# Kernel optimization log

Hardware: AMD Instinct MI355X
Metric: run time of the kernel (lower is better)

## Reference

```python
import jax, jax.numpy as jnp
import numpy as np

PAD = 200000   # padding index = all_features_num
D = 128        # input_dim (embedding dim)
H = 256        # hidden_dim
K = 15         # item_num (top-k)
M = 4          # multi_head


def _cos(a, b, eps=1e-8):
    # torch.cosine_similarity semantics with eps clamp on norms
    na = jnp.maximum(jnp.linalg.norm(a, axis=-1), eps)
    nb = jnp.maximum(jnp.linalg.norm(b, axis=-1), eps)
    return jnp.sum(a * b, axis=-1) / (na * nb)


def _rnn_input(x, emb):
    # x: [..., T, F] int. Fields :-2 are embedded+summed, field -2 is time.
    t = x[..., -2].astype(jnp.float32)
    dt = jnp.concatenate([jnp.zeros_like(t[..., :1]), jnp.diff(t, axis=-1)], axis=-1)
    e = emb[x[..., :-2]].sum(axis=-2)          # [..., T, D]
    x_self = e[:, 0:1, -1:, :]                  # [B,1,1,D] (self item placed at last slot of session 0)
    return jnp.concatenate([e, dt[..., None]], axis=-1), x_self


def _time_rnn(seq, W, U, b, wt, return_all=False):
    # Time-aware GRU. seq: [N, T, in+1]; last channel is delta-time feeding a decay gate.
    f, dt = seq[..., :-1], seq[..., -1:]
    N = seq.shape[0]
    g_in = jnp.einsum('nti,ij->ntj', f, W) + b   # precompute input projections [N,T,3H]

    def step(h, inp):
        g, d = inp                               # g:[N,3H], d:[N,1]
        decay = jnp.exp(-jax.nn.relu(d * wt))    # time-aware decay of hidden state
        hd = h * decay
        u = hd @ U
        z = jax.nn.sigmoid(g[:, :H] + u[:, :H])
        r = jax.nn.sigmoid(g[:, H:2 * H] + u[:, H:2 * H])
        n = jnp.tanh(g[:, 2 * H:] + r * u[:, 2 * H:])
        h_new = (1.0 - z) * hd + z * n
        return h_new, h_new

    h0 = jnp.zeros((N, H), seq.dtype)
    h_last, hs = jax.lax.scan(step, h0, (jnp.swapaxes(g_in, 0, 1), jnp.swapaxes(dt, 0, 1)))
    return jnp.swapaxes(hs, 0, 1) if return_all else h_last


def setup_inputs() -> dict:
    key = jax.random.key(0)
    ks = jax.random.split(key, 20)
    def n(k, shape, s=0.05):
        return jax.random.normal(k, shape, jnp.float32) * s
    x = jax.random.randint(ks[0], (512, 16, 64, 8), 0, PAD, dtype=jnp.int32)
    x_continuous = jax.random.randint(ks[1], (128, 128, 8), 0, PAD, dtype=jnp.int32)
    self_loc = jax.random.randint(ks[2], (512,), 0, 64, dtype=jnp.int32)
    emb = n(ks[3], (PAD + 1, D)).at[PAD].set(0.0)  # padding_idx row = 0
    return {
        'x': x, 'x_continuous': x_continuous, 'self_loc': self_loc, 'emb': emb,
        'W_rnn': n(ks[4], (2 * D, 3 * H)), 'U_rnn': n(ks[5], (H, 3 * H)), 'b_rnn': n(ks[6], (3 * H,)),
        'wt_rnn': jax.random.uniform(ks[7], (H,), jnp.float32, 0.0, 1e-5),
        'W_c': n(ks[8], (D, 3 * H)), 'U_c': n(ks[9], (H, 3 * H)), 'b_c': n(ks[10], (3 * H,)),
        'wt_c': jax.random.uniform(ks[11], (H,), jnp.float32, 0.0, 1e-5),
        'Wv': n(ks[12], (2 * H, M)), 'bv': n(ks[13], (M,)),
        'W0': n(ks[14], (D + (2 + M) * H, 1024)), 'b0': n(ks[15], (1024,)),
        'W1': n(ks[16], (1024, 512)), 'b1': n(ks[17], (512,)),
        'W2': n(ks[18], (512, 256)), 'b2': n(ks[19], (256,)),
        'Wp': n(jax.random.fold_in(key, 99), (256, 1)), 'bp': jnp.zeros((1,), jnp.float32),
    }


def reference(x, x_continuous, self_loc, emb, W_rnn, U_rnn, b_rnn, wt_rnn,
              W_c, U_c, b_c, wt_c, Wv, bv, W0, b0, W1, b1, W2, b2, Wp, bp):
    B = x.shape[0]
    label_len = B // x_continuous.shape[0]
    # ---- get_top_k: cosine sim + topk + gather ----
    real = x[..., 0] != PAD                         # [B,S,L]
    bidx = jnp.arange(B)
    e_self = emb[x[bidx, 0, self_loc, -3]]           # [B,D]
    e_items = emb[x[..., -3]]                        # [B,S,L,D]
    cos = _cos(e_self[:, None, None, :], e_items)    # [B,S,L]
    neg = jnp.min(jnp.where(real, cos, jnp.inf)) - 1.0
    sim = jnp.where(real, cos, neg)
    top_idx = jnp.sort(jax.lax.top_k(sim, K)[1], axis=-1)      # [B,S,K]
    x_top = jnp.take_along_axis(x, top_idx[..., None], axis=2)  # [B,S,K,F]
    x_top = x_top.at[:, 0, -1].set(x[bidx, 0, self_loc])
    # ---- rnn inputs ----
    xs, x_self = _rnn_input(x_top, emb)              # [B,S,K,D+1], [B,1,1,D]
    xs = jnp.concatenate([jnp.broadcast_to(x_self, xs.shape[:-1] + (D,)), xs], axis=-1)
    xs = xs.reshape(-1, K, 2 * D + 1)                # [B*S,K,2D+1]
    xc, _ = _rnn_input(x_continuous[:, None], emb)
    xc = xc[:, 0]                                    # [B',L2,D+1]
    # ---- RNNs ----
    h = _time_rnn(xs, W_rnn, U_rnn, b_rnn, wt_rnn).reshape(B, -1, H)   # [B,S,H]
    h_cont = _time_rnn(xc, W_c, U_c, b_c, wt_c, return_all=True)[:, -label_len:, :].reshape(B, H)
    # ---- multi-head attention over sessions ----
    a1 = jnp.concatenate([h, jnp.broadcast_to(h[:, :1], h.shape)], axis=-1) @ Wv + bv  # [B,S,M]
    a2 = jax.nn.softmax(jnp.tanh(a1), axis=1)
    h_att = jnp.einsum('bsm,bsh->bmh', a2, h).reshape(B, M * H)
    hh = jnp.concatenate([x_self.reshape(B, D), h[:, 0], h_att, h_cont], axis=-1)
    # ---- predict MLP (dropout = identity in eval) ----
    lr = lambda v: jnp.where(v > 0, v, 0.01 * v)     # LeakyReLU(0.01)
    z = lr(hh @ W0 + b0)
    z = lr(z @ W1 + b1)
    z = lr(z @ W2 + b2)
    return jax.nn.sigmoid(z @ Wp + bp)               # [B,1]
```

## Files before the change

kernel.cpp:

```cpp
#include <hip/hip_runtime.h>
#include <hip/hip_bf16.h>


#define PAD_TOK 200000
#define DD 128
#define HH 256
#define KK 15
#define BB 512
#define SS 16
#define II 64

typedef __bf16 bf16x8 __attribute__((ext_vector_type(8)));
typedef __bf16 bf16x4 __attribute__((ext_vector_type(4)));
typedef float f32x4 __attribute__((ext_vector_type(4)));
#define MFMA16 __builtin_amdgcn_mfma_f32_16x16x32_bf16
#define MFMA8 __builtin_amdgcn_mfma_f32_16x16x32_fp8_fp8

__device__ __forceinline__ float sigm(float x) { return 1.f / (1.f + __expf(-x)); }
__device__ __forceinline__ float tanh_fast(float x) {
  x = fminf(fmaxf(x, -15.f), 15.f);
  float e2 = __expf(2.f * x);
  return (e2 - 1.f) / (e2 + 1.f);
}
__device__ __forceinline__ float bfu(unsigned u16) { return __uint_as_float(u16 << 16); }

__device__ __forceinline__ unsigned char f2fp8(float x) {
  unsigned u = __float_as_uint(x);
  unsigned s = (u >> 31) << 7;
  int e = (int)((u >> 23) & 0xff) - 127;
  if (e < -6) return (unsigned char)s;
  unsigned m = (u >> 20) & 7;
  unsigned rest = u & 0xFFFFF;
  if (rest > 0x80000 || (rest == 0x80000 && (m & 1))) {
    ++m;
    if (m == 8) {
      m = 0;
      ++e;
    }
  }
  if (e > 7) {
    e = 7;
    m = 6;
  }
  return (unsigned char)(s | ((unsigned)(e + 7) << 3) | m);
}

__device__ __forceinline__ unsigned cvt2fp8(float a, float b) {
#if __has_builtin(__builtin_amdgcn_cvt_pk_fp8_f32)
  return (unsigned)__builtin_amdgcn_cvt_pk_fp8_f32(a, b, 0, false) & 0xffffu;
#else
  return (unsigned)f2fp8(a) | ((unsigned)f2fp8(b) << 8);
#endif
}

__global__ __launch_bounds__(128) void k_eself(const int* __restrict__ x,
                                               const int* __restrict__ self_loc,
                                               const float* __restrict__ emb,
                                               float* __restrict__ es,
                                               float* __restrict__ ns) {
  int b = blockIdx.x, d = threadIdx.x;
  int tok = x[((size_t)(b * SS + 0) * II + self_loc[b]) * 8 + 5];
  float v = emb[(size_t)tok * DD + d];
  es[b * DD + d] = v;
  __shared__ float red[128];
  red[d] = v * v;
  __syncthreads();
  for (int o = 64; o > 0; o >>= 1) {
    if (d < o) red[d] += red[d + o];
    __syncthreads();
  }
  if (d == 0) ns[b] = fmaxf(sqrtf(red[0]), 1e-8f);
}

__global__ void k_init(unsigned* minu) { *minu = 0xFFFFFFFFu; }

__global__ __launch_bounds__(256) void k_cos(const int* __restrict__ x,
                                             const float* __restrict__ emb,
                                             const float* __restrict__ es,
                                             const float* __restrict__ ns,
                                             float* __restrict__ simw,
                                             unsigned* __restrict__ minu) {
  int row = blockIdx.x;
  int b = row >> 4;
  int tid = threadIdx.x;
  int i = tid >> 2;
  int q = tid & 3;
  __shared__ float esl[128];
  __shared__ unsigned smin[64];
  if (tid < 128) esl[tid] = es[b * DD + tid];
  __syncthreads();
  const int* xr = x + ((size_t)row * II + i) * 8;
  int tok = xr[5];
  int first = xr[0];
  const float4* ep = (const float4*)(emb + (size_t)tok * DD + q * 32);
  const float4* sp = (const float4*)(esl + q * 32);
  float dot = 0.f, ss = 0.f;
#pragma unroll
  for (int j = 0; j < 8; ++j) {
    float4 a = ep[j];
    float4 e = sp[j];
    dot += a.x * e.x + a.y * e.y + a.z * e.z + a.w * e.w;
    ss += a.x * a.x + a.y * a.y + a.z * a.z + a.w * a.w;
  }
  dot += __shfl_xor(dot, 1);
  ss += __shfl_xor(ss, 1);
  dot += __shfl_xor(dot, 2);
  ss += __shfl_xor(ss, 2);
  if (q == 0) {
    float cosv = dot / (fmaxf(sqrtf(ss), 1e-8f) * ns[b]);
    simw[(size_t)row * II + i] = cosv;
    unsigned key = 0xFFFFFFFFu;
    if (first != PAD_TOK) {
      unsigned u = __float_as_uint(cosv);
      key = (cosv < 0.f) ? ~u : (u | 0x80000000u);
    }
    smin[i] = key;
  }
  __syncthreads();
  if (tid < 64) {
    unsigned m = smin[tid];
    for (int o = 32; o; o >>= 1) m = min(m, __shfl_xor(m, o));
    if (tid == 0 && m != 0xFFFFFFFFu) atomicMin(minu, m);
  }
}

__global__ __launch_bounds__(64) void k_topk(const int* __restrict__ x,
                                             const float* __restrict__ simw,
                                             const unsigned* __restrict__ minu,
                                             int* __restrict__ topidx) {
  int row = blockIdx.x, i = threadIdx.x;
  unsigned mk = *minu;
  float neg = ((mk & 0x80000000u) ? __uint_as_float(mk ^ 0x80000000u) : __uint_as_float(~mk)) - 1.0f;
  float c = simw[(size_t)row * II + i];
  bool real = x[((size_t)row * II + i) * 8] != PAD_TOK;
  float s = real ? c : neg;
  __shared__ float sv[64];
  sv[i] = s;
  __syncthreads();
  int rank = 0;
  for (int j = 0; j < 64; ++j) {
    float o = sv[j];
    rank += (o > s) || (o == s && j < i);
  }
  bool sel = rank < KK;
  unsigned long long mask = __ballot(sel);
  if (sel) {
    int pos = __popcll(mask & ((1ull << i) - 1ull));
    topidx[row * KK + pos] = i;
  }
}

__global__ __launch_bounds__(256) void k_build_main(const int* __restrict__ x,
                                                    const int* __restrict__ self_loc,
                                                    const float* __restrict__ emb,
                                                    const int* __restrict__ topidx,
                                                    __bf16* __restrict__ em,
                                                    float* __restrict__ dtm,
                                                    float* __restrict__ xself,
                                                    __bf16* __restrict__ xself_bf) {
  int t = blockIdx.y;
  int n = blockIdx.x * 8 + (threadIdx.x >> 5);
  int q = threadIdx.x & 31;
  int b = n >> 4, s = n & 15;
  bool ovr = (s == 0) && (t == KK - 1);
  int item = ovr ? self_loc[b] : topidx[n * KK + t];
  const int* xr = x + ((size_t)n * II + item) * 8;
  int toks[6];
#pragma unroll
  for (int jj = 0; jj < 6; ++jj) toks[jj] = xr[jj];
  float4 acc = {0.f, 0.f, 0.f, 0.f};
#pragma unroll
  for (int jj = 0; jj < 6; ++jj) {
    float4 v = *(const float4*)(emb + (size_t)toks[jj] * DD + q * 4);
    acc.x += v.x;
    acc.y += v.y;
    acc.z += v.z;
    acc.w += v.w;
  }
  bf16x4 ov = {(__bf16)acc.x, (__bf16)acc.y, (__bf16)acc.z, (__bf16)acc.w};
  *(bf16x4*)(em + ((size_t)t * 8192 + n) * DD + q * 4) = ov;
  if (ovr) {
    *(float4*)(xself + b * DD + q * 4) = acc;
    *(bf16x4*)(xself_bf + b * DD + q * 4) = ov;
  }
  if (q == 0) {
    float dtv = 0.f;
    if (t > 0) {
      int pitem = topidx[n * KK + t - 1];
      dtv = (float)xr[6] - (float)x[((size_t)n * II + pitem) * 8 + 6];
    }
    dtm[t * 8192 + n] = dtv;
  }
}

__global__ __launch_bounds__(128) void k_build_cont(const int* __restrict__ xc,
                                                    const float* __restrict__ emb,
                                                    __hip_bfloat16* __restrict__ ec,
                                                    float* __restrict__ dtc) {
  int p = blockIdx.x, t = blockIdx.y, d = threadIdx.x;
  const int* xr = xc + ((size_t)p * 128 + t) * 8;
  float acc = 0.f;
#pragma unroll
  for (int jj = 0; jj < 6; ++jj) acc += emb[(size_t)xr[jj] * DD + d];
  ec[((size_t)p * 128 + t) * DD + d] = __float2bfloat16(acc);
  if (d == 0) dtc[p * 128 + t] = (t > 0) ? ((float)xr[6] - (float)xr[-2]) : 0.f;
}

__global__ __launch_bounds__(64) void k_pack(const float* __restrict__ B,
                                             __bf16* __restrict__ out) {
  int kt = blockIdx.x, tile = blockIdx.y, lane = threadIdx.x;
  const float* src = B + (size_t)(kt * 32 + (lane >> 4) * 8) * 768 + tile * 16 + (lane & 15);
  __bf16* o = out + (((size_t)(kt * 48 + tile) * 64 + lane) * 8);
#pragma unroll
  for (int i = 0; i < 8; ++i) o[i] = (__bf16)src[(size_t)i * 768];
}

__global__ __launch_bounds__(64) void k_pack8(const float* __restrict__ B,
                                              unsigned char* __restrict__ out) {
  int kt = blockIdx.x, tile = blockIdx.y, lane = threadIdx.x;
  const float* src = B + (size_t)(kt * 32 + (lane >> 4) * 8) * 768 + tile * 16 + (lane & 15);
  unsigned char* o = out + (((size_t)(kt * 48 + tile) * 64 + lane) * 8);
#pragma unroll
  for (int i = 0; i < 8; ++i) o[i] = f2fp8(src[(size_t)i * 768] * 8.f);
}

__global__ __launch_bounds__(64) void k_packN(const float* __restrict__ B,
                                              __bf16* __restrict__ out, int N) {
  int kt = blockIdx.x, tile = blockIdx.y, lane = threadIdx.x;
  const float* src = B + (size_t)(kt * 32 + (lane >> 4) * 8) * N + tile * 16 + (lane & 15);
  __bf16* o = out + (((size_t)kt * gridDim.y + tile) * 64 + lane) * 8;
#pragma unroll
  for (int i = 0; i < 8; ++i) o[i] = (__bf16)src[(size_t)i * N];
}

__global__ __launch_bounds__(512) void k_gemm_g(const __hip_bfloat16* __restrict__ A,
                                                const __bf16* __restrict__ pB,
                                                const float* __restrict__ bias,
                                                __bf16* __restrict__ G2) {
  const int wv = threadIdx.x >> 6, lane = threadIdx.x & 63;
  const int lr = lane & 15, lg = lane >> 4;
  const int r0 = blockIdx.x * 32;
  f32x4 z4 = {0.f, 0.f, 0.f, 0.f};
  f32x4 acc[2][6];
#pragma unroll
  for (int mt = 0; mt < 2; ++mt)
#pragma unroll
    for (int n = 0; n < 6; ++n) acc[mt][n] = z4;
#pragma unroll
  for (int kt = 0; kt < 4; ++kt) {
    bf16x8 a[2];
#pragma unroll
    for (int mt = 0; mt < 2; ++mt)
      a[mt] = *(const bf16x8*)(A + (size_t)(r0 + mt * 16 + lr) * 128 + kt * 32 + lg * 8);
#pragma unroll
    for (int n = 0; n < 6; ++n) {
      bf16x8 b = *(const bf16x8*)(pB + (((size_t)kt * 48 + wv * 6 + n) * 64 + lane) * 8);
      acc[0][n] = MFMA16(a[0], b, acc[0][n], 0, 0, 0);
      acc[1][n] = MFMA16(a[1], b, acc[1][n], 0, 0, 0);
    }
  }
#pragma unroll
  for (int mt = 0; mt < 2; ++mt)
#pragma unroll
    for (int n = 0; n < 6; ++n) {
      int col = wv * 96 + n * 16 + lr;
      int gate = col >> 8, wvc = (col >> 5) & 7, nt = (col >> 4) & 1;
      float bc = bias[col];
#pragma unroll
      for (int r = 0; r < 4; ++r) {
        int row = r0 + mt * 16 + lg * 4 + r;
        G2[(size_t)row * 1024 + wvc * 128 + lr * 8 + gate * 2 + nt] = (__bf16)(acc[mt][n][r] + bc);
      }
    }
}

__device__ void cont_body(char* smem, const __bf16* __restrict__ G2,
                          const float* __restrict__ dtc,
                          const unsigned char* __restrict__ pU8,
                          const float* __restrict__ wt, float* __restrict__ hcont,
                          int blk) {
  unsigned char(*hbuf)[16 * 256] = (unsigned char(*)[16 * 256])smem;
  unsigned char(*uL)[30 * 512] = (unsigned char(*)[30 * 512])(smem + 8192);
  float* dl = (float*)(smem + 8192 + 122880);
  const int wv = threadIdx.x >> 6, lane = threadIdx.x & 63;
  const int lr = lane & 15, lg = lane >> 4;
  const int p0 = blk * 16;
  for (int idx = threadIdx.x; idx < 2048; idx += 512)
    dl[idx] = dtc[(p0 + (idx >> 7)) * 128 + (idx & 127)];
  for (int i = threadIdx.x; i < 8 * 30 * 64; i += 512) {
    int l = i & 63;
    int fw = i >> 6;
    int f = fw % 30;
    int w = fw / 30;
    int kt = 3 + f / 6;
    int gi = f % 6;
    *(uint2*)&uL[w][(size_t)f * 512 + l * 8] =
        *(const uint2*)(pU8 + (((size_t)kt * 48 + (gi >> 1) * 16 + w * 2 + (gi & 1)) * 64 + l) * 8);
  }
  long fr[3][6];
#pragma unroll
  for (int kt = 0; kt < 3; ++kt)
#pragma unroll
    for (int gi = 0; gi < 6; ++gi)
      fr[kt][gi] =
          *(const long*)(pU8 + (((size_t)kt * 48 + (gi >> 1) * 16 + wv * 2 + (gi & 1)) * 64 + lane) * 8);

  float wtv[2];
#pragma unroll
  for (int nt = 0; nt < 2; ++nt) wtv[nt] = wt[wv * 32 + nt * 16 + lr];
  float h[2][4];
#pragma unroll
  for (int nt = 0; nt < 2; ++nt)
#pragma unroll
    for (int r = 0; r < 4; ++r) h[nt][r] = 0.f;

  const uint4* G2v = (const uint4*)G2;
  const size_t gb0 = (size_t)(p0 + lg * 4) * 16384 + wv * 16 + lr;
  __syncthreads();

  for (int t = 0; t < 128; ++t) {
    unsigned char* hb = hbuf[t & 1];
    uint4 Gv[4];
#pragma unroll
    for (int r = 0; r < 4; ++r) Gv[r] = G2v[gb0 + (size_t)r * 16384 + (size_t)t * 128];
    float hd[2][4];
#pragma unroll
    for (int r = 0; r < 4; ++r) {
      float dtv = dl[(lg * 4 + r) * 128 + t];
#pragma unroll
      for (int nt = 0; nt < 2; ++nt) hd[nt][r] = h[nt][r] * __expf(-fmaxf(dtv * wtv[nt], 0.f));
    }
    const int c0 = wv * 32 + lr, c1 = wv * 32 + 16 + lr;
#pragma unroll
    for (int r = 0; r < 4; ++r) {
      int row = lg * 4 + r;
      int sw = (row & 15) << 3;
      unsigned pk = cvt2fp8(hd[0][r] * 16.f, hd[1][r] * 16.f);
      hb[row * 256 + (c0 ^ sw)] = (unsigned char)pk;
      hb[row * 256 + (c1 ^ sw)] = (unsigned char)(pk >> 8);
    }
    __syncthreads();
    f32x4 acc[3][2];
#pragma unroll
    for (int g = 0; g < 3; ++g)
#pragma unroll
      for (int nt = 0; nt < 2; ++nt) acc[g][nt] = f32x4{0.f, 0.f, 0.f, 0.f};
#pragma unroll
    for (int kt = 0; kt < 8; ++kt) {
      long a = *(const long*)&hb[lr * 256 + ((kt * 32 + lg * 8) ^ ((lr & 15) << 3))];
#pragma unroll
      for (int gi = 0; gi < 6; ++gi) {
        long b = (kt < 3) ? fr[kt][gi]
                          : *(const long*)&uL[wv][(size_t)((kt - 3) * 6 + gi) * 512 + lane * 8];
        acc[gi >> 1][gi & 1] = MFMA8(a, b, acc[gi >> 1][gi & 1], 0, 0, 0);
      }
    }
#pragma unroll
    for (int nt = 0; nt < 2; ++nt)
#pragma unroll
      for (int r = 0; r < 4; ++r) {
        unsigned uz = nt ? (Gv[r].x >> 16) : (Gv[r].x & 0xffffu);
        unsigned ur = nt ? (Gv[r].y >> 16) : (Gv[r].y & 0xffffu);
        unsigned un = nt ? (Gv[r].z >> 16) : (Gv[r].z & 0xffffu);
        const float us = 0.0078125f;
        float zz = sigm(bfu(uz) + acc[0][nt][r] * us);
        float rr = sigm(bfu(ur) + acc[1][nt][r] * us);
        float nn = tanh_fast(bfu(un) + rr * acc[2][nt][r] * us);
        float hnew = (1.f - zz) * hd[nt][r] + zz * nn;
        h[nt][r] = hnew;
        if (t >= 124)
          hcont[((size_t)(p0 + lg * 4 + r) * 4 + (t - 124)) * 256 + wv * 32 + nt * 16 + lr] = hnew;
      }
  }
}

__device__ void main_body(char* smem, const __bf16* __restrict__ em,
                          const float* __restrict__ dtm,
                          const __bf16* __restrict__ xself_bf,
                          const __bf16* __restrict__ pWs, const __bf16* __restrict__ pWe,
                          const __bf16* __restrict__ pU, const float* __restrict__ bg,
                          const float* __restrict__ wt, float* __restrict__ hmain,
                          int blk) {
  __bf16(*hbuf)[32 * 256] = (__bf16(*)[32 * 256])smem;
  float* dl = (float*)(smem + 32768);
  const int wv = threadIdx.x >> 6, lane = threadIdx.x & 63;
  const int lr = lane & 15, lg = lane >> 4;
  const int n0 = blk * 32;
  f32x4 z4 = {0.f, 0.f, 0.f, 0.f};
  for (int idx = threadIdx.x; idx < KK * 32; idx += 512)
    dl[idx] = dtm[(idx >> 5) * 8192 + n0 + (idx & 31)];
  float wtv[2], bz[2], br[2], bn[2];
#pragma unroll
  for (int nt = 0; nt < 2; ++nt) {
    int c = wv * 32 + nt * 16 + lr;
    wtv[nt] = wt[c];
    bz[nt] = bg[c];
    br[nt] = bg[c + 256];
    bn[nt] = bg[c + 512];
  }
  float h[2][2][4];
#pragma unroll
  for (int mt = 0; mt < 2; ++mt)
#pragma unroll
    for (int nt = 0; nt < 2; ++nt)
#pragma unroll
      for (int r = 0; r < 4; ++r) h[mt][nt][r] = 0.f;
  __syncthreads();

  for (int t = 0; t < KK; ++t) {
    __bf16* hb = hbuf[t & 1];
#pragma unroll
    for (int mt = 0; mt < 2; ++mt)
#pragma unroll
      for (int r = 0; r < 4; ++r) {
        float dtv = dl[t * 32 + mt * 16 + lg * 4 + r];
        int row = mt * 16 + lg * 4 + r;
#pragma unroll
        for (int nt = 0; nt < 2; ++nt) {
          float hdv = h[mt][nt][r] * __expf(-fmaxf(dtv * wtv[nt], 0.f));
          hb[((row * 256) + (wv * 32 + nt * 16 + lr)) ^ ((row & 7) << 3)] = (__bf16)hdv;
        }
      }
    __syncthreads();

#pragma unroll
    for (int ntp = 0; ntp < 2; ++ntp) {
      f32x4 acc[4][2];
#pragma unroll
      for (int a4 = 0; a4 < 4; ++a4)
#pragma unroll
        for (int mt = 0; mt < 2; ++mt) acc[a4][mt] = z4;
#pragma unroll 2
      for (int kt = 0; kt < 8; ++kt) {
        bf16x8 a[2];
#pragma unroll
        for (int mt = 0; mt < 2; ++mt) {
          int row = mt * 16 + lr;
          int s = ((row * 256) + (kt * 32 + lg * 8)) ^ ((row & 7) << 3);
          a[mt] = *(const bf16x8*)&hb[s];
        }
#pragma unroll
        for (int g = 0; g < 3; ++g) {
          const int ai = (g < 2) ? g : 3;
          bf16x8 b = *(const bf16x8*)(pU + (((size_t)kt * 48 + g * 16 + wv * 2 + ntp) * 64 + lane) * 8);
#pragma unroll
          for (int mt = 0; mt < 2; ++mt) acc[ai][mt] = MFMA16(a[mt], b, acc[ai][mt], 0, 0, 0);
        }
      }
#pragma unroll 2
      for (int kt = 0; kt < 8; ++kt) {
        bf16x8 a[2];
#pragma unroll
        for (int mt = 0; mt < 2; ++mt) {
          if (kt < 4)
            a[mt] = *(const bf16x8*)(xself_bf + (size_t)((n0 + mt * 16) >> 4) * 128 + kt * 32 + lg * 8);
          else
            a[mt] = *(const bf16x8*)(em + ((size_t)t * 8192 + n0 + mt * 16 + lr) * 128 +
                                     (kt - 4) * 32 + lg * 8);
        }
        const __bf16* pB = (kt < 4) ? (pWs + (size_t)kt * 48 * 512)
                                    : (pWe + (size_t)(kt - 4) * 48 * 512);
#pragma unroll
        for (int g = 0; g < 3; ++g) {
          bf16x8 b = *(const bf16x8*)(pB + (((size_t)g * 16 + wv * 2 + ntp) * 64 + lane) * 8);
#pragma unroll
          for (int mt = 0; mt < 2; ++mt) acc[g][mt] = MFMA16(a[mt], b, acc[g][mt], 0, 0, 0);
        }
      }
#pragma unroll
      for (int mt = 0; mt < 2; ++mt)
#pragma unroll
        for (int r = 0; r < 4; ++r) {
          float dtv = dl[t * 32 + mt * 16 + lg * 4 + r];
          float hdv = h[mt][ntp][r] * __expf(-fmaxf(dtv * wtv[ntp], 0.f));
          float zz = sigm(acc[0][mt][r] + bz[ntp]);
          float rr = sigm(acc[1][mt][r] + br[ntp]);
          float nn = tanh_fast(acc[2][mt][r] + bn[ntp] + rr * acc[3][mt][r]);
          h[mt][ntp][r] = (1.f - zz) * hdv + zz * nn;
        }
    }
  }
  __syncthreads();
#pragma unroll
  for (int mt = 0; mt < 2; ++mt)
#pragma unroll
    for (int nt = 0; nt < 2; ++nt)
#pragma unroll
      for (int r = 0; r < 4; ++r)
        hmain[(size_t)(n0 + mt * 16 + lg * 4 + r) * 256 + wv * 32 + nt * 16 + lr] = h[mt][nt][r];
}

__global__ __launch_bounds__(512) void k_rnn_fused(
    const __bf16* __restrict__ G2, const float* __restrict__ dtc,
    const unsigned char* __restrict__ pU8, const float* __restrict__ wt_c,
    float* __restrict__ hcont, const __bf16* __restrict__ em,
    const float* __restrict__ dtm, const __bf16* __restrict__ xself_bf,
    const __bf16* __restrict__ pWs, const __bf16* __restrict__ pWe,
    const __bf16* __restrict__ pU, const float* __restrict__ b_rnn,
    const float* __restrict__ wt_m, float* __restrict__ hmain) {
  __shared__ __align__(16) char smem[8192 + 122880 + 8192];
  if (blockIdx.x < 8)
    cont_body(smem, G2, dtc, pU8, wt_c, hcont, blockIdx.x);
  else
    main_body(smem, em, dtm, xself_bf, pWs, pWe, pU, b_rnn, wt_m, hmain, blockIdx.x - 8);
}

__global__ __launch_bounds__(256) void k_att(const float* __restrict__ hmain,
                                             const float* __restrict__ xself,
                                             const float* __restrict__ hc,
                                             const float* __restrict__ Wv,
                                             const float* __restrict__ bv,
                                             float* __restrict__ hh,
                                             __bf16* __restrict__ hh_bf) {
  int b = blockIdx.x, tid = threadIdx.x;
  __shared__ float hl[16 * 256];
  __shared__ float aa[16 * 4];
  for (int idx = tid; idx < 4096; idx += 256) hl[idx] = hmain[(size_t)b * SS * HH + idx];
  __syncthreads();
  if (tid < 64) {
    int s = tid >> 2, m = tid & 3;
    float acc = bv[m];
    for (int j = 0; j < 256; ++j)
      acc += hl[s * 256 + j] * Wv[j * 4 + m] + hl[j] * Wv[(256 + j) * 4 + m];
    aa[s * 4 + m] = tanh_fast(acc);
  }
  __syncthreads();
  if (tid < 4) {
    int m = tid;
    float mx = -1e30f;
    for (int s = 0; s < 16; ++s) mx = fmaxf(mx, aa[s * 4 + m]);
    float sum = 0.f;
    for (int s = 0; s < 16; ++s) sum += __expf(aa[s * 4 + m] - mx);
    float inv = 1.f / sum;
    for (int s = 0; s < 16; ++s) aa[s * 4 + m] = __expf(aa[s * 4 + m] - mx) * inv;
  }
  __syncthreads();
  float a0 = 0.f, a1 = 0.f, a2 = 0.f, a3 = 0.f;
  for (int s = 0; s < 16; ++s) {
    float hv = hl[s * 256 + tid];
    a0 = fmaf(aa[s * 4 + 0], hv, a0);
    a1 = fmaf(aa[s * 4 + 1], hv, a1);
    a2 = fmaf(aa[s * 4 + 2], hv, a2);
    a3 = fmaf(aa[s * 4 + 3], hv, a3);
  }
  float* hb = hh + (size_t)b * 1664;
  __bf16* hf = hh_bf + (size_t)b * 1664;
  hb[384 + 0 * 256 + tid] = a0;
  hb[384 + 1 * 256 + tid] = a1;
  hb[384 + 2 * 256 + tid] = a2;
  hb[384 + 3 * 256 + tid] = a3;
  hf[384 + 0 * 256 + tid] = (__bf16)a0;
  hf[384 + 1 * 256 + tid] = (__bf16)a1;
  hf[384 + 2 * 256 + tid] = (__bf16)a2;
  hf[384 + 3 * 256 + tid] = (__bf16)a3;
  if (tid < 128) {
    hb[tid] = xself[b * DD + tid];
    hf[tid] = (__bf16)xself[b * DD + tid];
  }
  hb[128 + tid] = hl[tid];
  hf[128 + tid] = (__bf16)hl[tid];
  float hcv = hc[(size_t)b * HH + tid];
  hb[1408 + tid] = hcv;
  hf[1408 + tid] = (__bf16)hcv;
}

__global__ __launch_bounds__(512) void k_mlp_mfma(const __bf16* __restrict__ A,
                                                  const __bf16* __restrict__ pW,
                                                  const float* __restrict__ bias,
                                                  __bf16* __restrict__ C, int K, int N) {
  const int wv = threadIdx.x >> 6, lane = threadIdx.x & 63;
  const int lr = lane & 15, lg = lane >> 4;
  const int r0 = blockIdx.y * 32;
  const int c0 = blockIdx.x * 256;
  const int NT = N >> 4;
  const int KT = K >> 5;
  f32x4 acc[2][2];
#pragma unroll
  for (int mt = 0; mt < 2; ++mt)
#pragma unroll
    for (int nt = 0; nt < 2; ++nt) acc[mt][nt] = f32x4{0.f, 0.f, 0.f, 0.f};
  for (int kt = 0; kt < KT; ++kt) {
    bf16x8 a[2];
#pragma unroll
    for (int mt = 0; mt < 2; ++mt)
      a[mt] = *(const bf16x8*)(A + (size_t)(r0 + mt * 16 + lr) * K + kt * 32 + lg * 8);
#pragma unroll
    for (int nt = 0; nt < 2; ++nt) {
      bf16x8 b = *(const bf16x8*)(pW + (((size_t)kt * NT + (c0 >> 4) + wv * 2 + nt) * 64 + lane) * 8);
#pragma unroll
      for (int mt = 0; mt < 2; ++mt) acc[mt][nt] = MFMA16(a[mt], b, acc[mt][nt], 0, 0, 0);
    }
  }
#pragma unroll
  for (int nt = 0; nt < 2; ++nt) {
    int col = c0 + wv * 32 + nt * 16 + lr;
    float bc = bias[col];
#pragma unroll
    for (int mt = 0; mt < 2; ++mt)
#pragma unroll
      for (int r = 0; r < 4; ++r) {
        float v = acc[mt][nt][r] + bc;
        v = v > 0.f ? v : 0.01f * v;
        C[(size_t)(r0 + mt * 16 + lg * 4 + r) * N + col] = (__bf16)v;
      }
  }
}

__global__ __launch_bounds__(64) void k_head(const __bf16* __restrict__ A,
                                             const float* __restrict__ Wp,
                                             const float* __restrict__ bp,
                                             float* __restrict__ out) {
  int row = blockIdx.x, l = threadIdx.x;
  float acc = 0.f;
  for (int j = l; j < 256; j += 64) acc = fmaf((float)A[(size_t)row * 256 + j], Wp[j], acc);
  for (int o = 32; o; o >>= 1) acc += __shfl_xor(acc, o);
  if (l == 0) out[row] = 1.f / (1.f + __expf(-(acc + bp[0])));
}

extern "C" void kernel_launch(void* const* d_in, const int* in_sizes, int n_in,
                              void* d_out, int out_size, void* d_ws, size_t ws_size,
                              hipStream_t stream) {
  const int* x = (const int*)d_in[0];
  const int* xc = (const int*)d_in[1];
  const int* self_loc = (const int*)d_in[2];
  const float* emb = (const float*)d_in[3];
  const float* W_rnn = (const float*)d_in[4];
  const float* U_rnn = (const float*)d_in[5];
  const float* b_rnn = (const float*)d_in[6];
  const float* wt_rnn = (const float*)d_in[7];
  const float* W_c = (const float*)d_in[8];
  const float* U_c = (const float*)d_in[9];
  const float* b_c = (const float*)d_in[10];
  const float* wt_c = (const float*)d_in[11];
  const float* Wv = (const float*)d_in[12];
  const float* bv = (const float*)d_in[13];
  const float* W0 = (const float*)d_in[14];
  const float* b0 = (const float*)d_in[15];
  const float* W1 = (const float*)d_in[16];
  const float* b1 = (const float*)d_in[17];
  const float* W2 = (const float*)d_in[18];
  const float* b2 = (const float*)d_in[19];
  const float* Wp = (const float*)d_in[20];
  const float* bp = (const float*)d_in[21];
  float* out = (float*)d_out;

  char* ws = (char*)d_ws;
  size_t cur = 0;
  auto alloc = [&](size_t bytes) {
    char* p = ws + cur;
    cur += (bytes + 255) & ~(size_t)255;
    return p;
  };
  float* es = (float*)alloc((size_t)BB * DD * 4);
  float* ns = (float*)alloc(BB * 4);
  unsigned* minu = (unsigned*)alloc(4);
  float* simw = (float*)alloc((size_t)BB * SS * II * 4);
  int* topidx = (int*)alloc((size_t)BB * SS * KK * 4);
  float* xself = (float*)alloc((size_t)BB * DD * 4);
  __bf16* xself_bf = (__bf16*)alloc((size_t)BB * DD * 2);
  float* dtm = (float*)alloc((size_t)KK * 8192 * 4);
  float* dtc = (float*)alloc((size_t)128 * 128 * 4);
  float* hcont = (float*)alloc((size_t)BB * HH * 4);
  float* hh = (float*)alloc((size_t)BB * 1664 * 4);
  __bf16* hh_bf = (__bf16*)alloc((size_t)BB * 1664 * 2);
  __bf16* z0 = (__bf16*)alloc((size_t)BB * 1024 * 2);
  __bf16* z1 = (__bf16*)alloc((size_t)BB * 512 * 2);
  __bf16* z2 = (__bf16*)alloc((size_t)BB * 256 * 2);
  float* hmain = (float*)alloc((size_t)8192 * HH * 4);
  __hip_bfloat16* ec = (__hip_bfloat16*)alloc((size_t)16384 * DD * 2);
  __bf16* em = (__bf16*)alloc((size_t)KK * 8192 * DD * 2);
  __bf16* G2 = (__bf16*)alloc((size_t)16384 * 1024 * 2);
  __bf16* pWs = (__bf16*)alloc((size_t)4 * 48 * 64 * 8 * 2);
  __bf16* pWe = (__bf16*)alloc((size_t)4 * 48 * 64 * 8 * 2);
  __bf16* pU = (__bf16*)alloc((size_t)8 * 48 * 64 * 8 * 2);
  __bf16* pWc = (__bf16*)alloc((size_t)4 * 48 * 64 * 8 * 2);
  unsigned char* pU8 = (unsigned char*)alloc((size_t)8 * 48 * 64 * 8);
  __bf16* pW0 = (__bf16*)alloc((size_t)52 * 64 * 64 * 8 * 2);
  __bf16* pW1 = (__bf16*)alloc((size_t)32 * 32 * 64 * 8 * 2);
  __bf16* pW2 = (__bf16*)alloc((size_t)16 * 16 * 64 * 8 * 2);
  (void)ws_size;

  hipLaunchKernelGGL(k_init, dim3(1), dim3(1), 0, stream, minu);
  hipLaunchKernelGGL(k_eself, dim3(BB), dim3(128), 0, stream, x, self_loc, emb, es, ns);
  hipLaunchKernelGGL(k_cos, dim3(BB * SS), dim3(256), 0, stream, x, emb, es, ns, simw, minu);
  hipLaunchKernelGGL(k_topk, dim3(BB * SS), dim3(64), 0, stream, x, simw, minu, topidx);
  hipLaunchKernelGGL(k_build_main, dim3(1024, KK), dim3(256), 0, stream, x, self_loc, emb,
                     topidx, em, dtm, xself, xself_bf);
  hipLaunchKernelGGL(k_build_cont, dim3(128, 128), dim3(128), 0, stream, xc, emb, ec, dtc);
  hipLaunchKernelGGL(k_pack, dim3(4, 48), dim3(64), 0, stream, W_rnn, pWs);
  hipLaunchKernelGGL(k_pack, dim3(4, 48), dim3(64), 0, stream, W_rnn + 128 * 768, pWe);
  hipLaunchKernelGGL(k_pack, dim3(8, 48), dim3(64), 0, stream, U_rnn, pU);
  hipLaunchKernelGGL(k_pack, dim3(4, 48), dim3(64), 0, stream, W_c, pWc);
  hipLaunchKernelGGL(k_pack8, dim3(8, 48), dim3(64), 0, stream, U_c, pU8);
  hipLaunchKernelGGL(k_packN, dim3(52, 64), dim3(64), 0, stream, W0, pW0, 1024);
  hipLaunchKernelGGL(k_packN, dim3(32, 32), dim3(64), 0, stream, W1, pW1, 512);
  hipLaunchKernelGGL(k_packN, dim3(16, 16), dim3(64), 0, stream, W2, pW2, 256);
  hipLaunchKernelGGL(k_gemm_g, dim3(512), dim3(512), 0, stream, ec, pWc, b_c, G2);
  hipLaunchKernelGGL(k_rnn_fused, dim3(264), dim3(512), 0, stream, G2, dtc, pU8, wt_c,
                     hcont, em, dtm, xself_bf, pWs, pWe, pU, b_rnn, wt_rnn, hmain);
  hipLaunchKernelGGL(k_att, dim3(BB), dim3(256), 0, stream, hmain, xself, hcont, Wv, bv, hh,
                     hh_bf);
  hipLaunchKernelGGL(k_mlp_mfma, dim3(4, 16), dim3(512), 0, stream, hh_bf, pW0, b0, z0,
                     1664, 1024);
  hipLaunchKernelGGL(k_mlp_mfma, dim3(2, 16), dim3(512), 0, stream, z0, pW1, b1, z1, 1024,
                     512);
  hipLaunchKernelGGL(k_mlp_mfma, dim3(1, 16), dim3(512), 0, stream, z1, pW2, b2, z2, 512,
                     256);
  hipLaunchKernelGGL(k_head, dim3(BB), dim3(64), 0, stream, z2, Wp, bp, out);
}
```

Baseline: 774.4 us.

## Fuse cosine top-k selection and main embedding build into RNN blocks

Removes the separate self-embedding, cosine-similarity, top-k and main-sequence build kernels. Each main RNN block now computes these for its own 32 rows in shared memory before running the recurrence. This drops several launches and global round-trips for the similarity, top-k index and delta-time buffers, and lets this gather work overlap with the long continuous-RNN blocks. The global atomic-min used to pick a padding score is replaced by a constant -3, which still ranks below any cosine value. In exchange, the gather work now runs on only 256 blocks instead of large grids. The main-path embeddings are still written to and re-read from global memory.

```diff
diff --git a/kernel.cpp b/kernel.cpp
--- a/kernel.cpp
+++ b/kernel.cpp
@@ -51,146 +51,6 @@
 #else
   return (unsigned)f2fp8(a) | ((unsigned)f2fp8(b) << 8);
 #endif
-}
-
-__global__ __launch_bounds__(128) void k_eself(const int* __restrict__ x,
-                                               const int* __restrict__ self_loc,
-                                               const float* __restrict__ emb,
-                                               float* __restrict__ es,
-                                               float* __restrict__ ns) {
-  int b = blockIdx.x, d = threadIdx.x;
-  int tok = x[((size_t)(b * SS + 0) * II + self_loc[b]) * 8 + 5];
-  float v = emb[(size_t)tok * DD + d];
-  es[b * DD + d] = v;
-  __shared__ float red[128];
-  red[d] = v * v;
-  __syncthreads();
-  for (int o = 64; o > 0; o >>= 1) {
-    if (d < o) red[d] += red[d + o];
-    __syncthreads();
-  }
-  if (d == 0) ns[b] = fmaxf(sqrtf(red[0]), 1e-8f);
-}
-
-__global__ void k_init(unsigned* minu) { *minu = 0xFFFFFFFFu; }
-
-__global__ __launch_bounds__(256) void k_cos(const int* __restrict__ x,
-                                             const float* __restrict__ emb,
-                                             const float* __restrict__ es,
-                                             const float* __restrict__ ns,
-                                             float* __restrict__ simw,
-                                             unsigned* __restrict__ minu) {
-  int row = blockIdx.x;
-  int b = row >> 4;
-  int tid = threadIdx.x;
-  int i = tid >> 2;
-  int q = tid & 3;
-  __shared__ float esl[128];
-  __shared__ unsigned smin[64];
-  if (tid < 128) esl[tid] = es[b * DD + tid];
-  __syncthreads();
-  const int* xr = x + ((size_t)row * II + i) * 8;
-  int tok = xr[5];
-  int first = xr[0];
-  const float4* ep = (const float4*)(emb + (size_t)tok * DD + q * 32);
-  const float4* sp = (const float4*)(esl + q * 32);
-  float dot = 0.f, ss = 0.f;
-#pragma unroll
-  for (int j = 0; j < 8; ++j) {
-    float4 a = ep[j];
-    float4 e = sp[j];
-    dot += a.x * e.x + a.y * e.y + a.z * e.z + a.w * e.w;
-    ss += a.x * a.x + a.y * a.y + a.z * a.z + a.w * a.w;
-  }
-  dot += __shfl_xor(dot, 1);
-  ss += __shfl_xor(ss, 1);
-  dot += __shfl_xor(dot, 2);
-  ss += __shfl_xor(ss, 2);
-  if (q == 0) {
-    float cosv = dot / (fmaxf(sqrtf(ss), 1e-8f) * ns[b]);
-    simw[(size_t)row * II + i] = cosv;
-    unsigned key = 0xFFFFFFFFu;
-    if (first != PAD_TOK) {
-      unsigned u = __float_as_uint(cosv);
-      key = (cosv < 0.f) ? ~u : (u | 0x80000000u);
-    }
-    smin[i] = key;
-  }
-  __syncthreads();
-  if (tid < 64) {
-    unsigned m = smin[tid];
-    for (int o = 32; o; o >>= 1) m = min(m, __shfl_xor(m, o));
-    if (tid == 0 && m != 0xFFFFFFFFu) atomicMin(minu, m);
-  }
-}
-
-__global__ __launch_bounds__(64) void k_topk(const int* __restrict__ x,
-                                             const float* __restrict__ simw,
-                                             const unsigned* __restrict__ minu,
-                                             int* __restrict__ topidx) {
-  int row = blockIdx.x, i = threadIdx.x;
-  unsigned mk = *minu;
-  float neg = ((mk & 0x80000000u) ? __uint_as_float(mk ^ 0x80000000u) : __uint_as_float(~mk)) - 1.0f;
-  float c = simw[(size_t)row * II + i];
-  bool real = x[((size_t)row * II + i) * 8] != PAD_TOK;
-  float s = real ? c : neg;
-  __shared__ float sv[64];
-  sv[i] = s;
-  __syncthreads();
-  int rank = 0;
-  for (int j = 0; j < 64; ++j) {
-    float o = sv[j];
-    rank += (o > s) || (o == s && j < i);
-  }
-  bool sel = rank < KK;
-  unsigned long long mask = __ballot(sel);
-  if (sel) {
-    int pos = __popcll(mask & ((1ull << i) - 1ull));
-    topidx[row * KK + pos] = i;
-  }
-}
-
-__global__ __launch_bounds__(256) void k_build_main(const int* __restrict__ x,
-                                                    const int* __restrict__ self_loc,
-                                                    const float* __restrict__ emb,
-                                                    const int* __restrict__ topidx,
-                                                    __bf16* __restrict__ em,
-                                                    float* __restrict__ dtm,
-                                                    float* __restrict__ xself,
-                                                    __bf16* __restrict__ xself_bf) {
-  int t = blockIdx.y;
-  int n = blockIdx.x * 8 + (threadIdx.x >> 5);
-  int q = threadIdx.x & 31;
-  int b = n >> 4, s = n & 15;
-  bool ovr = (s == 0) && (t == KK - 1);
-  int item = ovr ? self_loc[b] : topidx[n * KK + t];
-  const int* xr = x + ((size_t)n * II + item) * 8;
-  int toks[6];
-#pragma unroll
-  for (int jj = 0; jj < 6; ++jj) toks[jj] = xr[jj];
-  float4 acc = {0.f, 0.f, 0.f, 0.f};
-#pragma unroll
-  for (int jj = 0; jj < 6; ++jj) {
-    float4 v = *(const float4*)(emb + (size_t)toks[jj] * DD + q * 4);
-    acc.x += v.x;
-    acc.y += v.y;
-    acc.z += v.z;
-    acc.w += v.w;
-  }
-  bf16x4 ov = {(__bf16)acc.x, (__bf16)acc.y, (__bf16)acc.z, (__bf16)acc.w};
-  *(bf16x4*)(em + ((size_t)t * 8192 + n) * DD + q * 4) = ov;
-  if (ovr) {
-    *(float4*)(xself + b * DD + q * 4) = acc;
-    *(bf16x4*)(xself_bf + b * DD + q * 4) = ov;
-  }
-  if (q == 0) {
-    float dtv = 0.f;
-    if (t > 0) {
-      int pitem = topidx[n * KK + t - 1];
-      dtv = (float)xr[6] - (float)x[((size_t)n * II + pitem) * 8 + 6];
-    }
-    dtm[t * 8192 + n] = dtv;
-  }
 }
 
 __global__ __launch_bounds__(128) void k_build_cont(const int* __restrict__ xc,
@@ -374,21 +234,122 @@
   }
 }
 
-__device__ void main_body(char* smem, const __bf16* __restrict__ em,
-                          const float* __restrict__ dtm,
-                          const __bf16* __restrict__ xself_bf,
+__device__ void main_body(char* smem, const int* __restrict__ x,
+                          const int* __restrict__ self_loc,
+                          const float* __restrict__ emb,
                           const __bf16* __restrict__ pWs, const __bf16* __restrict__ pWe,
                           const __bf16* __restrict__ pU, const float* __restrict__ bg,
-                          const float* __restrict__ wt, float* __restrict__ hmain,
+                          const float* __restrict__ wt, __bf16* __restrict__ em,
+                          float* __restrict__ xself, float* __restrict__ hmain,
                           int blk) {
   __bf16(*hbuf)[32 * 256] = (__bf16(*)[32 * 256])smem;
   float* dl = (float*)(smem + 32768);
-  const int wv = threadIdx.x >> 6, lane = threadIdx.x & 63;
+  float* esL = (float*)(smem + 34944);
+  float* nsL = (float*)(smem + 35968);
+  __bf16* xsbf = (__bf16*)(smem + 36000);
+  float* simL = (float*)(smem + 36544);
+  int* tpxL = (int*)(smem + 44736);
+  const int tid = threadIdx.x;
+  const int wv = tid >> 6, lane = tid & 63;
   const int lr = lane & 15, lg = lane >> 4;
   const int n0 = blk * 32;
+  const int b0 = n0 >> 4;
   f32x4 z4 = {0.f, 0.f, 0.f, 0.f};
-  for (int idx = threadIdx.x; idx < KK * 32; idx += 512)
-    dl[idx] = dtm[(idx >> 5) * 8192 + n0 + (idx & 31)];
+
+  if (tid < 256) {
+    int bb = tid >> 7, d = tid & 127;
+    int bgl = b0 + bb;
+    int tok = x[((size_t)(bgl * SS) * II + self_loc[bgl]) * 8 + 5];
+    esL[bb * 128 + d] = emb[(size_t)tok * DD + d];
+  }
+  __syncthreads();
+  if (tid < 128) {
+    int bb = tid >> 6, l = tid & 63;
+    float v0 = esL[bb * 128 + l], v1 = esL[bb * 128 + 64 + l];
+    float ss = v0 * v0 + v1 * v1;
+    for (int o = 32; o; o >>= 1) ss += __shfl_xor(ss, o);
+    if (l == 0) nsL[bb] = fmaxf(sqrtf(ss), 1e-8f);
+  }
+  __syncthreads();
+  for (int it = 0; it < 16; ++it) {
+    int pr = it * 128 + (tid >> 2);
+    int row = pr >> 6, item = pr & 63, q = tid & 3;
+    const int* xr = x + ((size_t)(n0 + row) * II + item) * 8;
+    int tok = xr[5];
+    int first = xr[0];
+    const float4* ep = (const float4*)(emb + (size_t)tok * DD + q * 32);
+    const float4* sp = (const float4*)(esL + (row >> 4) * 128 + q * 32);
+    float dot = 0.f, ss = 0.f;
+#pragma unroll
+    for (int j = 0; j < 8; ++j) {
+      float4 a = ep[j];
+      float4 e = sp[j];
+      dot += a.x * e.x + a.y * e.y + a.z * e.z + a.w * e.w;
+      ss += a.x * a.x + a.y * a.y + a.z * a.z + a.w * a.w;
+    }
+    dot += __shfl_xor(dot, 1);
+    ss += __shfl_xor(ss, 1);
+    dot += __shfl_xor(dot, 2);
+    ss += __shfl_xor(ss, 2);
+    if (q == 0)
+      simL[row * 64 + item] =
+          (first != PAD_TOK) ? dot / (fmaxf(sqrtf(ss), 1e-8f) * nsL[row >> 4]) : -3.0f;
+  }
+  __syncthreads();
+  for (int it = 0; it < 4; ++it) {
+    int pr = it * 512 + tid;
+    int row = pr >> 6, item = pr & 63;
+    float s = simL[row * 64 + item];
+    int rank = 0;
+    for (int j = 0; j < 64; ++j) {
+      float o = simL[row * 64 + j];
+      rank += (o > s) || (o == s && j < item);
+    }
+    bool sel = rank < KK;
+    unsigned long long mask = __ballot(sel);
+    if (sel) {
+      int pos = __popcll(mask & ((1ull << item) - 1ull));
+      tpxL[row * KK + pos] = item;
+    }
+  }
+  __syncthreads();
+  for (int t = 0; t < KK; ++t) {
+    int rr = tid >> 5, q = tid & 31;
+#pragma unroll
+    for (int pass = 0; pass < 2; ++pass) {
+      int rloc = pass * 16 + rr;
+      int ng = n0 + rloc;
+      int bb = ng >> 4, s = ng & 15;
+      bool ovr = (s == 0) && (t == KK - 1);
+      int item = ovr ? self_loc[bb] : tpxL[rloc * KK + t];
+      const int* xr = x + ((size_t)ng * II + item) * 8;
+      float4 a4 = {0.f, 0.f, 0.f, 0.f};
+#pragma unroll
+      for (int jj = 0; jj < 6; ++jj) {
+        float4 v = *(const float4*)(emb + (size_t)xr[jj] * DD + q * 4);
+        a4.x += v.x;
+        a4.y += v.y;
+        a4.z += v.z;
+        a4.w += v.w;
+      }
+      bf16x4 ov = {(__bf16)a4.x, (__bf16)a4.y, (__bf16)a4.z, (__bf16)a4.w};
+      *(bf16x4*)(em + ((size_t)t * 8192 + ng) * DD + q * 4) = ov;
+      if (ovr) {
+        *(float4*)(xself + bb * DD + q * 4) = a4;
+        *(bf16x4*)(xsbf + (bb - b0) * 128 + q * 4) = ov;
+      }
+      if (q == 0) {
+        float dtv = 0.f;
+        if (t > 0) {
+          int pitem = tpxL[rloc * KK + t - 1];
+          dtv = (float)xr[6] - (float)x[((size_t)ng * II + pitem) * 8 + 6];
+        }
+        dl[t * 32 + rloc] = dtv;
+      }
+    }
+  }
+  __syncthreads();
+
   float wtv[2], bz[2], br[2], bn[2];
 #pragma unroll
   for (int nt = 0; nt < 2; ++nt) {
@@ -405,7 +366,6 @@
     for (int nt = 0; nt < 2; ++nt)
 #pragma unroll
       for (int r = 0; r < 4; ++r) h[mt][nt][r] = 0.f;
-  __syncthreads();
 
   for (int t = 0; t < KK; ++t) {
     __bf16* hb = hbuf[t & 1];
@@ -422,7 +382,6 @@
         }
       }
     __syncthreads();
-
 #pragma unroll
     for (int ntp = 0; ntp < 2; ++ntp) {
       f32x4 acc[4][2];
@@ -453,7 +412,7 @@
 #pragma unroll
         for (int mt = 0; mt < 2; ++mt) {
           if (kt < 4)
-            a[mt] = *(const bf16x8*)(xself_bf + (size_t)((n0 + mt * 16) >> 4) * 128 + kt * 32 + lg * 8);
+            a[mt] = *(const bf16x8*)(xsbf + mt * 128 + kt * 32 + lg * 8);
           else
             a[mt] = *(const bf16x8*)(em + ((size_t)t * 8192 + n0 + mt * 16 + lr) * 128 +
                                      (kt - 4) * 32 + lg * 8);
@@ -493,16 +452,18 @@
 __global__ __launch_bounds__(512) void k_rnn_fused(
     const __bf16* __restrict__ G2, const float* __restrict__ dtc,
     const unsigned char* __restrict__ pU8, const float* __restrict__ wt_c,
-    float* __restrict__ hcont, const __bf16* __restrict__ em,
-    const float* __restrict__ dtm, const __bf16* __restrict__ xself_bf,
+    float* __restrict__ hcont, const int* __restrict__ x,
+    const int* __restrict__ self_loc, const float* __restrict__ emb,
     const __bf16* __restrict__ pWs, const __bf16* __restrict__ pWe,
     const __bf16* __restrict__ pU, const float* __restrict__ b_rnn,
-    const float* __restrict__ wt_m, float* __restrict__ hmain) {
+    const float* __restrict__ wt_m, __bf16* __restrict__ em,
+    float* __restrict__ xself, float* __restrict__ hmain) {
   __shared__ __align__(16) char smem[8192 + 122880 + 8192];
   if (blockIdx.x < 8)
     cont_body(smem, G2, dtc, pU8, wt_c, hcont, blockIdx.x);
   else
-    main_body(smem, em, dtm, xself_bf, pWs, pWe, pU, b_rnn, wt_m, hmain, blockIdx.x - 8);
+    main_body(smem, x, self_loc, emb, pWs, pWe, pU, b_rnn, wt_m, em, xself, hmain,
+              blockIdx.x - 8);
 }
 
 __global__ __launch_bounds__(256) void k_att(const float* __restrict__ hmain,
@@ -651,14 +612,7 @@
     cur += (bytes + 255) & ~(size_t)255;
     return p;
   };
-  float* es = (float*)alloc((size_t)BB * DD * 4);
-  float* ns = (float*)alloc(BB * 4);
-  unsigned* minu = (unsigned*)alloc(4);
-  float* simw = (float*)alloc((size_t)BB * SS * II * 4);
-  int* topidx = (int*)alloc((size_t)BB * SS * KK * 4);
   float* xself = (float*)alloc((size_t)BB * DD * 4);
-  __bf16* xself_bf = (__bf16*)alloc((size_t)BB * DD * 2);
-  float* dtm = (float*)alloc((size_t)KK * 8192 * 4);
   float* dtc = (float*)alloc((size_t)128 * 128 * 4);
   float* hcont = (float*)alloc((size_t)BB * HH * 4);
   float* hh = (float*)alloc((size_t)BB * 1664 * 4);
@@ -680,24 +634,19 @@
   __bf16* pW2 = (__bf16*)alloc((size_t)16 * 16 * 64 * 8 * 2);
   (void)ws_size;
 
-  hipLaunchKernelGGL(k_init, dim3(1), dim3(1), 0, stream, minu);
-  hipLaunchKernelGGL(k_eself, dim3(BB), dim3(128), 0, stream, x, self_loc, emb, es, ns);
-  hipLaunchKernelGGL(k_cos, dim3(BB * SS), dim3(256), 0, stream, x, emb, es, ns, simw, minu);
-  hipLaunchKernelGGL(k_topk, dim3(BB * SS), dim3(64), 0, stream, x, simw, minu, topidx);
-  hipLaunchKernelGGL(k_build_main, dim3(1024, KK), dim3(256), 0, stream, x, self_loc, emb,
-                     topidx, em, dtm, xself, xself_bf);
   hipLaunchKernelGGL(k_build_cont, dim3(128, 128), dim3(128), 0, stream, xc, emb, ec, dtc);
+  hipLaunchKernelGGL(k_pack, dim3(4, 48), dim3(64), 0, stream, W_c, pWc);
+  hipLaunchKernelGGL(k_pack8, dim3(8, 48), dim3(64), 0, stream, U_c, pU8);
+  hipLaunchKernelGGL(k_gemm_g, dim3(512), dim3(512), 0, stream, ec, pWc, b_c, G2);
   hipLaunchKernelGGL(k_pack, dim3(4, 48), dim3(64), 0, stream, W_rnn, pWs);
   hipLaunchKernelGGL(k_pack, dim3(4, 48), dim3(64), 0, stream, W_rnn + 128 * 768, pWe);
   hipLaunchKernelGGL(k_pack, dim3(8, 48), dim3(64), 0, stream, U_rnn, pU);
-  hipLaunchKernelGGL(k_pack, dim3(4, 48), dim3(64), 0, stream, W_c, pWc);
-  hipLaunchKernelGGL(k_pack8, dim3(8, 48), dim3(64), 0, stream, U_c, pU8);
   hipLaunchKernelGGL(k_packN, dim3(52, 64), dim3(64), 0, stream, W0, pW0, 1024);
   hipLaunchKernelGGL(k_packN, dim3(32, 32), dim3(64), 0, stream, W1, pW1, 512);
   hipLaunchKernelGGL(k_packN, dim3(16, 16), dim3(64), 0, stream, W2, pW2, 256);
-  hipLaunchKernelGGL(k_gemm_g, dim3(512), dim3(512), 0, stream, ec, pWc, b_c, G2);
   hipLaunchKernelGGL(k_rnn_fused, dim3(264), dim3(512), 0, stream, G2, dtc, pU8, wt_c,
-                     hcont, em, dtm, xself_bf, pWs, pWe, pU, b_rnn, wt_rnn, hmain);
+                     hcont, x, self_loc, emb, pWs, pWe, pU, b_rnn, wt_rnn, em, xself,
+                     hmain);
   hipLaunchKernelGGL(k_att, dim3(BB), dim3(256), 0, stream, hmain, xself, hcont, Wv, bv, hh,
                      hh_bf);
   hipLaunchKernelGGL(k_mlp_mfma, dim3(4, 16), dim3(512), 0, stream, hh_bf, pW0, b0, z0,
```

Result: no change. 766.1 us (-1.1%).
